# Kernel tuning notes

Measured on AMD Instinct MI355X. Metric: run time of the kernel, lower is better.

Reference implementation:

```python
import jax, jax.numpy as jnp
import numpy as np

N_ENT = 20000
N_REL = 24
N_EDGE = 200000
BATCH = 64
N_RULES = 32
RULE_LEN = 2


def setup_inputs() -> dict:
    key = jax.random.key(0)
    ks = jax.random.split(key, 9)
    return {
        "all_h": jax.random.randint(ks[0], (BATCH,), 0, N_ENT, dtype=jnp.int32),
        "all_r": jnp.zeros((BATCH,), dtype=jnp.int32),  # query relation = 0 for all queries
        "edges_to_remove": jax.random.randint(ks[1], (BATCH,), 0, N_EDGE, dtype=jnp.int32),
        "edge_heads": jax.random.randint(ks[2], (N_EDGE,), 0, N_ENT, dtype=jnp.int32),
        "edge_rels": jax.random.randint(ks[3], (N_EDGE,), 0, N_REL, dtype=jnp.int32),
        "edge_tails": jax.random.randint(ks[4], (N_EDGE,), 0, N_ENT, dtype=jnp.int32),
        "rule_bodies": jax.random.randint(ks[5], (N_RULES, RULE_LEN), 0, N_REL, dtype=jnp.int32),
        "rule_weights": jax.random.normal(ks[6], (N_RULES,), dtype=jnp.float32),
        "bias": jax.random.normal(ks[7], (N_ENT,), dtype=jnp.float32),
    }


def reference(all_h, all_r, edges_to_remove, edge_heads, edge_rels, edge_tails,
              rule_bodies, rule_weights, bias):
    n_ent = bias.shape[0]
    rule_len = rule_bodies.shape[1]
    b = all_h.shape[0]

    # edge keep-mask (edges_to_remove are dropped from the graph for this query batch)
    keep = jnp.ones((edge_heads.shape[0],), jnp.float32).at[edges_to_remove].set(0.0)

    # grounding start state: one-hot of query heads, [B, N]
    x0 = jax.nn.one_hot(all_h, n_ent, dtype=jnp.float32)

    def propagate(x, r):
        # one hop of rule grounding: route counts along edges with relation r
        w = keep * (edge_rels == r).astype(jnp.float32)      # [E]
        contrib = x[:, edge_heads] * w[None, :]              # [B, E] gather
        # scatter-add into tail entities -> [B, N]
        return jax.ops.segment_sum(contrib.T, edge_tails, num_segments=n_ent).T

    def per_rule(carry, rule):
        score, mask = carry
        body, weight = rule
        x = x0
        for l in range(rule_len):
            x = propagate(x, body[l])
        return (score + x * weight, mask + x), None

    zeros = jnp.zeros((b, n_ent), jnp.float32)
    (score, mask), _ = jax.lax.scan(per_rule, (zeros, zeros), (rule_bodies, rule_weights))

    # entity_feature == 'bias' path: score + bias, mask all True.
    # (If mask.sum()==0, score is also all-zero, so score+bias == mask+bias and
    #  (1-mask).bool() == ones: the two torch branches coincide for 'bias'.)
    out_score = score + bias[None, :]
    out_mask = jnp.ones_like(mask, dtype=bool)
    return out_score, out_mask
```

## Files before the change

### kernel.cpp

```cpp
#include <hip/hip_runtime.h>


namespace {
constexpr int kNEnt    = 20000;
constexpr int kNRel    = 24;
constexpr int kNEdge   = 200000;
constexpr int kBatch   = 64;
constexpr int kNRules  = 32;
constexpr int kWSz     = kNRel * kNRel;
constexpr int kScore4  = kBatch * kNEnt / 4;
constexpr int kOut4    = 2 * kScore4;
constexpr int kB1      = 1024;
constexpr int kT       = 256;
}

__global__ void __launch_bounds__(kT) k_init_frontier(
        const int* __restrict__ all_h,
        const int* __restrict__ rem,
        const int* __restrict__ eh,
        const int* __restrict__ er,
        const int* __restrict__ et,
        const float* __restrict__ bias,
        float* __restrict__ out,
        int* __restrict__ headptr,
        unsigned* __restrict__ nodeNext,
        unsigned long long* __restrict__ nodeBm) {
    __shared__ int sh[kBatch];
    __shared__ int srem[kBatch];
    const int t = threadIdx.x;
    if (t < kBatch) sh[t] = all_h[t];
    else if (t < 2 * kBatch) srem[t - kBatch] = rem[t - kBatch];
    __syncthreads();
    const int gid = blockIdx.x * kT + t;
    constexpr int stride = kB1 * kT;

    for (int i = gid; i < kOut4; i += stride) {
        if (i < kScore4)
            ((float4*)out)[i] = ((const float4*)bias)[i % (kNEnt / 4)];
        else
            ((float4*)out)[i] = make_float4(1.f, 1.f, 1.f, 1.f);
    }

    for (int e = gid; e < kNEdge; e += stride) {
        int h = eh[e];
        unsigned long long bm = 0ull;
        for (int b = 0; b < kBatch; b++)
            bm |= (unsigned long long)(sh[b] == h) << b;
        if (!bm) continue;
        bool removed = false;
        for (int i = 0; i < kBatch; i++) removed |= (srem[i] == e);
        if (removed) continue;
        int tail = et[e];
        int r1   = er[e];
        int old  = atomicExch(&headptr[tail], e + 1);
        unsigned nxt = (old <= 0) ? 0u : (unsigned)old;
        nodeNext[e] = nxt | ((unsigned)r1 << 24);
        nodeBm[e]   = bm;
    }
}

__global__ void __launch_bounds__(kT) k_hop2(
        const int* __restrict__ rem,
        const int* __restrict__ eh,
        const int* __restrict__ er,
        const int* __restrict__ et,
        const int* __restrict__ rb,
        const float* __restrict__ rw,
        const int* __restrict__ headptr,
        const unsigned* __restrict__ nodeNext,
        const unsigned long long* __restrict__ nodeBm,
        float* __restrict__ out) {
    __shared__ float sW[kWSz];
    __shared__ int srem[kBatch];
    const int t = threadIdx.x;
    for (int i = t; i < kWSz; i += kT) sW[i] = 0.f;
    if (t < kBatch) srem[t] = rem[t];
    __syncthreads();
    if (t < kNRules)
        atomicAdd(&sW[rb[2 * t] * kNRel + rb[2 * t + 1]], rw[t]);
    __syncthreads();

    int e = blockIdx.x * kT + t;
    if (e >= kNEdge) return;
    int h = eh[e];
    int p = headptr[h];
    if (p <= 0) return;
    bool removed = false;
    for (int i = 0; i < kBatch; i++) removed |= (srem[i] == e);
    if (removed) return;
    int r2 = er[e];
    int t2 = et[e];
    while (p > 0) {
        int e1 = p - 1;
        unsigned nx           = nodeNext[e1];
        unsigned long long bm = nodeBm[e1];
        float w = sW[((nx >> 24) & 31u) * kNRel + r2];
        while (bm) {
            int b = __ffsll(bm) - 1;
            bm &= bm - 1;
            atomicAdd(&out[b * kNEnt + t2], w);
        }
        p = (int)(nx & 0xFFFFFFu);
    }
}

extern "C" void kernel_launch(void* const* d_in, const int* in_sizes, int n_in,
                              void* d_out, int out_size, void* d_ws, size_t ws_size,
                              hipStream_t stream) {
    const int*   all_h = (const int*)d_in[0];
    const int*   rem   = (const int*)d_in[2];
    const int*   eh    = (const int*)d_in[3];
    const int*   er    = (const int*)d_in[4];
    const int*   et    = (const int*)d_in[5];
    const int*   rb    = (const int*)d_in[6];
    const float* rw    = (const float*)d_in[7];
    const float* bias  = (const float*)d_in[8];
    float* out = (float*)d_out;

    char* ws = (char*)d_ws;
    int*                headptr  = (int*)(ws + 0);
    unsigned*           nodeNext = (unsigned*)(ws + 81920);
    unsigned long long* nodeBm   = (unsigned long long*)(ws + 881920);

    hipLaunchKernelGGL(k_init_frontier, dim3(kB1), dim3(kT), 0, stream,
                       all_h, rem, eh, er, et, bias, out,
                       headptr, nodeNext, nodeBm);
    hipLaunchKernelGGL(k_hop2, dim3((kNEdge + kT - 1) / kT), dim3(kT), 0, stream,
                       rem, eh, er, et, rb, rw, headptr, nodeNext, nodeBm, out);
}
```

Before: 83.65 us.

## Fuse frontier build and hop-2 scatter into one kernel with a grid barrier

Merges the frontier-init kernel and the hop-2 scatter kernel into a single persistent launch of 512 blocks. A hand-rolled grid-wide barrier, built from per-block flags with release/acquire atomics and s_sleep polling, separates the two phases. This removes one kernel launch and the gap between the two kernels. In exchange, all blocks must be co-resident and polling costs some time. The flags are written with a fixed magic value and never cleared, so unless the workspace is zeroed before each call, later calls can pass the barrier before the first phase has finished.

After: 180.4 us. 116% more time.

```diff
diff --git a/kernel.cpp b/kernel.cpp
--- a/kernel.cpp
+++ b/kernel.cpp
@@ -10,38 +10,48 @@
 constexpr int kWSz     = kNRel * kNRel;
 constexpr int kScore4  = kBatch * kNEnt / 4;
 constexpr int kOut4    = 2 * kScore4;
-constexpr int kB1      = 1024;
+constexpr int kBlocks  = 512;
 constexpr int kT       = 256;
+constexpr int kGrid    = kBlocks * kT;
+constexpr int kMagic   = 0x135A79;
 }
 
-__global__ void __launch_bounds__(kT) k_init_frontier(
+__global__ void __launch_bounds__(kT) k_fused(
         const int* __restrict__ all_h,
         const int* __restrict__ rem,
         const int* __restrict__ eh,
         const int* __restrict__ er,
         const int* __restrict__ et,
+        const int* __restrict__ rb,
+        const float* __restrict__ rw,
         const float* __restrict__ bias,
         float* __restrict__ out,
         int* __restrict__ headptr,
         unsigned* __restrict__ nodeNext,
-        unsigned long long* __restrict__ nodeBm) {
-    __shared__ int sh[kBatch];
-    __shared__ int srem[kBatch];
-    const int t = threadIdx.x;
-    if (t < kBatch) sh[t] = all_h[t];
-    else if (t < 2 * kBatch) srem[t - kBatch] = rem[t - kBatch];
+        unsigned long long* __restrict__ nodeBm,
+        int* __restrict__ flags) {
+    __shared__ int   sh[kBatch];
+    __shared__ int   srem[kBatch];
+    __shared__ float sW[kWSz];
+    const int t   = threadIdx.x;
+    const int bid = blockIdx.x;
+
+    for (int i = t; i < kWSz; i += kT) sW[i] = 0.f;
+    if (t < kBatch) { sh[t] = all_h[t]; srem[t] = rem[t]; }
     __syncthreads();
-    const int gid = blockIdx.x * kT + t;
-    constexpr int stride = kB1 * kT;
+    if (t < kNRules)
+        atomicAdd(&sW[rb[2 * t] * kNRel + rb[2 * t + 1]], rw[t]);
 
-    for (int i = gid; i < kOut4; i += stride) {
+    const int gid = bid * kT + t;
+
+    for (int i = gid; i < kOut4; i += kGrid) {
         if (i < kScore4)
             ((float4*)out)[i] = ((const float4*)bias)[i % (kNEnt / 4)];
         else
             ((float4*)out)[i] = make_float4(1.f, 1.f, 1.f, 1.f);
     }
 
-    for (int e = gid; e < kNEdge; e += stride) {
+    for (int e = gid; e < kNEdge; e += kGrid) {
         int h = eh[e];
         unsigned long long bm = 0ull;
         for (int b = 0; b < kBatch; b++)
@@ -57,50 +67,41 @@
         nodeNext[e] = nxt | ((unsigned)r1 << 24);
         nodeBm[e]   = bm;
     }
-}
 
-__global__ void __launch_bounds__(kT) k_hop2(
-        const int* __restrict__ rem,
-        const int* __restrict__ eh,
-        const int* __restrict__ er,
-        const int* __restrict__ et,
-        const int* __restrict__ rb,
-        const float* __restrict__ rw,
-        const int* __restrict__ headptr,
-        const unsigned* __restrict__ nodeNext,
-        const unsigned long long* __restrict__ nodeBm,
-        float* __restrict__ out) {
-    __shared__ float sW[kWSz];
-    __shared__ int srem[kBatch];
-    const int t = threadIdx.x;
-    for (int i = t; i < kWSz; i += kT) sW[i] = 0.f;
-    if (t < kBatch) srem[t] = rem[t];
+    __threadfence();
     __syncthreads();
-    if (t < kNRules)
-        atomicAdd(&sW[rb[2 * t] * kNRel + rb[2 * t + 1]], rw[t]);
+    if (t == 0)
+        __hip_atomic_store(&flags[bid], kMagic,
+                           __ATOMIC_RELEASE, __HIP_MEMORY_SCOPE_AGENT);
+    for (int j = t; j < kBlocks; j += kT) {
+        while (__hip_atomic_load(&flags[j],
+                                 __ATOMIC_ACQUIRE, __HIP_MEMORY_SCOPE_AGENT)
+               != kMagic)
+            __builtin_amdgcn_s_sleep(8);
+    }
     __syncthreads();
 
-    int e = blockIdx.x * kT + t;
-    if (e >= kNEdge) return;
-    int h = eh[e];
-    int p = headptr[h];
-    if (p <= 0) return;
-    bool removed = false;
-    for (int i = 0; i < kBatch; i++) removed |= (srem[i] == e);
-    if (removed) return;
-    int r2 = er[e];
-    int t2 = et[e];
-    while (p > 0) {
-        int e1 = p - 1;
-        unsigned nx           = nodeNext[e1];
-        unsigned long long bm = nodeBm[e1];
-        float w = sW[((nx >> 24) & 31u) * kNRel + r2];
-        while (bm) {
-            int b = __ffsll(bm) - 1;
-            bm &= bm - 1;
-            atomicAdd(&out[b * kNEnt + t2], w);
+    for (int e = gid; e < kNEdge; e += kGrid) {
+        int h = eh[e];
+        int p = headptr[h];
+        if (p <= 0) continue;
+        bool removed = false;
+        for (int i = 0; i < kBatch; i++) removed |= (srem[i] == e);
+        if (removed) continue;
+        int r2 = er[e];
+        int t2 = et[e];
+        while (p > 0) {
+            int e1 = p - 1;
+            unsigned nx           = nodeNext[e1];
+            unsigned long long bm = nodeBm[e1];
+            float w = sW[((nx >> 24) & 31u) * kNRel + r2];
+            while (bm) {
+                int b = __ffsll(bm) - 1;
+                bm &= bm - 1;
+                atomicAdd(&out[b * kNEnt + t2], w);
+            }
+            p = (int)(nx & 0xFFFFFFu);
         }
-        p = (int)(nx & 0xFFFFFFu);
     }
 }
 
@@ -121,10 +122,9 @@
     int*                headptr  = (int*)(ws + 0);
     unsigned*           nodeNext = (unsigned*)(ws + 81920);
     unsigned long long* nodeBm   = (unsigned long long*)(ws + 881920);
+    int*                flags    = (int*)(ws + 2481920);
 
-    hipLaunchKernelGGL(k_init_frontier, dim3(kB1), dim3(kT), 0, stream,
-                       all_h, rem, eh, er, et, bias, out,
-                       headptr, nodeNext, nodeBm);
-    hipLaunchKernelGGL(k_hop2, dim3((kNEdge + kT - 1) / kT), dim3(kT), 0, stream,
-                       rem, eh, er, et, rb, rw, headptr, nodeNext, nodeBm, out);
+    hipLaunchKernelGGL(k_fused, dim3(kBlocks), dim3(kT), 0, stream,
+                       all_h, rem, eh, er, et, rb, rw, bias, out,
+                       headptr, nodeNext, nodeBm, flags);
 }
```
